# Optimization experiments

Measured on AMD Instinct MI355X. Metric: run time of the kernel, lower is better.

## Reference

```python
import jax, jax.numpy as jnp
import numpy as np

ALPHA = 0.7
L_CHAMFER, L_EDGE, L_SMOOTH, L_NORMAL = 1.0, 2.0, 1.0, 0.5
EPS = 1e-8

N, M, P, G, F = 8192, 8192, 8192, 8192, 16384


def _cdist(a, b):
    # Euclidean distance matrix, (N,3) x (M,3) -> (N,M); matches torch.cdist
    d2 = (jnp.sum(a * a, axis=1)[:, None]
          + jnp.sum(b * b, axis=1)[None, :]
          - 2.0 * a @ b.T)
    return jnp.sqrt(jnp.maximum(d2, 0.0))


def _chamfer(a, b):
    d = _cdist(a, b)
    return (d.min(axis=1).mean() + d.min(axis=0).mean()) * 0.5


def _unit(x, key):
    v = jax.random.normal(key, x, dtype=jnp.float32)
    return v / jnp.linalg.norm(v, axis=1, keepdims=True)


def setup_inputs() -> dict:
    key = jax.random.key(0)
    ks = jax.random.split(key, 7)
    return {
        "student_verts": jax.random.normal(ks[0], (N, 3), dtype=jnp.float32),
        "student_normals": _unit((N, 3), ks[1]),
        "teacher_verts": jax.random.normal(ks[2], (M, 3), dtype=jnp.float32),
        "teacher_normals": _unit((M, 3), ks[3]),
        "teacher_points": jax.random.normal(ks[4], (P, 3), dtype=jnp.float32),
        "gt_points": jax.random.normal(ks[5], (G, 3), dtype=jnp.float32),
        "faces": jax.random.randint(ks[6], (F, 3), 0, N, dtype=jnp.int32),
    }


def reference(student_verts, student_normals, teacher_verts, teacher_normals,
              teacher_points, gt_points, faces):
    # --- chamfer losses ---
    loss_teacher = _chamfer(student_verts, teacher_points)
    loss_gt = _chamfer(student_verts, gt_points)
    loss_chamfer = ALPHA * loss_teacher + (1.0 - ALPHA) * loss_gt

    # --- mesh edge loss: mean squared edge length ---
    edges = jnp.concatenate([faces[:, [0, 1]], faces[:, [1, 2]], faces[:, [2, 0]]], axis=0)  # (3F,2)
    ev = student_verts[edges[:, 0]] - student_verts[edges[:, 1]]
    loss_edge = jnp.sum(ev * ev, axis=1).mean()

    # --- uniform laplacian smoothing: mean || mean(nbrs) - v || ---
    nverts = student_verts.shape[0]
    src = jnp.concatenate([edges[:, 0], edges[:, 1]])
    dst = jnp.concatenate([edges[:, 1], edges[:, 0]])
    nbr_sum = jax.ops.segment_sum(student_verts[dst], src, num_segments=nverts)
    deg = jax.ops.segment_sum(jnp.ones_like(src, dtype=jnp.float32), src, num_segments=nverts)
    lap = nbr_sum / jnp.maximum(deg, 1.0)[:, None] - student_verts
    loss_smooth = jnp.linalg.norm(lap, axis=1).mean()
    # replicate norm with safe sqrt for grad stability

    # --- normal loss via nearest teacher vertex ---
    d_tv = _cdist(student_verts, teacher_verts)  # (N,M)
    nearest_idx = jnp.argmin(d_tv, axis=1)
    target_normals = teacher_normals[nearest_idx]  # (N,3)
    num = jnp.sum(student_normals * target_normals, axis=1)
    den = (jnp.maximum(jnp.linalg.norm(student_normals, axis=1), EPS)
           * jnp.maximum(jnp.linalg.norm(target_normals, axis=1), EPS))
    loss_normal = 1.0 - (num / den).mean()

    total = (L_CHAMFER * loss_chamfer + L_EDGE * loss_edge
             + L_SMOOTH * loss_smooth + L_NORMAL * loss_normal)
    return total
```

## Files before the change

### kernel.cpp

```cpp
#include <hip/hip_runtime.h>


typedef float f32x2 __attribute__((ext_vector_type(2)));
typedef float f32x4 __attribute__((ext_vector_type(4)));

#define BLK 256
#define TA 8
#define JC 128
#define NJG (JC / 4)

__device__ __forceinline__ float wave_reduce_sum(float v) {
#pragma unroll
  for (int o = 32; o > 0; o >>= 1) v += __shfl_down(v, o, 64);
  return v;
}

__device__ __forceinline__ unsigned flipf(float f) {
  unsigned b = __float_as_uint(f);
  return (b & 0x80000000u) ? ~b : (b | 0x80000000u);
}
__device__ __forceinline__ float unflipf(unsigned u) {
  unsigned b = (u & 0x80000000u) ? (u ^ 0x80000000u) : ~u;
  return __uint_as_float(b);
}

__device__ __forceinline__ f32x2 splat2(float v) {
  f32x2 r; r.x = v; r.y = v; return r;
}

__global__ void init_ws_kernel(unsigned long long* __restrict__ min64, int n64,
                               unsigned* __restrict__ minbits, int nmin,
                               float* __restrict__ zr, int nz) {
  const int stride = gridDim.x * blockDim.x;
  const int t0 = blockIdx.x * blockDim.x + threadIdx.x;
  for (int i = t0; i < n64; i += stride) min64[i] = ~0ull;
  for (int i = t0; i < nmin; i += stride) minbits[i] = 0xFF800000u;
  for (int i = t0; i < nz; i += stride) zr[i] = 0.0f;
}

struct Desc {
  const float* A[5];
  const float* B[5];
  void* out[5];
  const int* fc; int f;
  const float* sv;
  float* nbr; float* deg; float* acc;
  int nRows, nCols;
};

#define DIST2(d01, d23, X_, Y_, Z_, W_, k)                                 \
  f32x2 d01 = __builtin_elementwise_fma(naz[k], (Z_).xy, (W_).xy);         \
  d01 = __builtin_elementwise_fma(nay[k], (Y_).xy, d01);                   \
  d01 = __builtin_elementwise_fma(nax[k], (X_).xy, d01);                   \
  f32x2 d23 = __builtin_elementwise_fma(naz[k], (Z_).zw, (W_).zw);         \
  d23 = __builtin_elementwise_fma(nay[k], (Y_).zw, d23);                   \
  d23 = __builtin_elementwise_fma(nax[k], (X_).zw, d23);

__global__ void __launch_bounds__(BLK) mega_kernel(Desc d) {
  const int pass = blockIdx.z;
  const int t = threadIdx.x;

  if (pass == 5) {
    const int nE = 3 * d.f;
    const int bid = blockIdx.y * gridDim.x + blockIdx.x;
    const int stride = gridDim.x * gridDim.y * BLK;
    float es = 0.f;
    for (int e = bid * BLK + t; e < nE; e += stride) {
      int a, b;
      if (e < d.f)          { a = d.fc[3 * e + 0];  b = d.fc[3 * e + 1]; }
      else if (e < 2 * d.f) { int q = e - d.f;     a = d.fc[3 * q + 1]; b = d.fc[3 * q + 2]; }
      else                  { int q = e - 2 * d.f; a = d.fc[3 * q + 2]; b = d.fc[3 * q + 0]; }
      float ax = d.sv[3 * a], ay = d.sv[3 * a + 1], az = d.sv[3 * a + 2];
      float bx = d.sv[3 * b], by = d.sv[3 * b + 1], bz = d.sv[3 * b + 2];
      float dx = ax - bx, dy = ay - by, dz = az - bz;
      es += fmaf(dx, dx, fmaf(dy, dy, dz * dz));
      atomicAdd(&d.nbr[3 * a + 0], bx);
      atomicAdd(&d.nbr[3 * a + 1], by);
      atomicAdd(&d.nbr[3 * a + 2], bz);
      atomicAdd(&d.nbr[3 * b + 0], ax);
      atomicAdd(&d.nbr[3 * b + 1], ay);
      atomicAdd(&d.nbr[3 * b + 2], az);
      atomicAdd(&d.deg[a], 1.0f);
      atomicAdd(&d.deg[b], 1.0f);
    }
    es = wave_reduce_sum(es);
    if ((t & 63) == 0) atomicAdd(&d.acc[4], es);
    return;
  }

  __shared__ f32x4 sX[NJG], sY[NJG], sZ[NJG], sW[NJG];
  const float* __restrict__ A = d.A[pass];
  const float* __restrict__ B = d.B[pass];
  const int j0 = blockIdx.y * JC;
  if (t < JC) {
    int j = j0 + t;
    float bx = 0.f, by = 0.f, bz = 0.f, bw = 1e30f;
    if (j < d.nCols) {
      bx = B[3 * j]; by = B[3 * j + 1]; bz = B[3 * j + 2];
      bw = fmaf(bx, bx, fmaf(by, by, bz * bz));
    }
    ((float*)sX)[t] = bx; ((float*)sY)[t] = by;
    ((float*)sZ)[t] = bz; ((float*)sW)[t] = bw;
  }

  const int rowBase = blockIdx.x * (TA * BLK) + t;
  f32x2 nax[TA], nay[TA], naz[TA], m2[TA];
#pragma unroll
  for (int k = 0; k < TA; ++k) {
    int r = rowBase + k * BLK;
    int rc = (r < d.nRows) ? r : 0;
    nax[k] = splat2(-2.0f * A[3 * rc + 0]);
    nay[k] = splat2(-2.0f * A[3 * rc + 1]);
    naz[k] = splat2(-2.0f * A[3 * rc + 2]);
    m2[k] = splat2(1e30f);
  }
  __syncthreads();

  if (pass < 4) {
    f32x4 X = sX[0], Y = sY[0], Z = sZ[0], W = sW[0];
#pragma unroll 2
    for (int jg = 0; jg < NJG - 1; ++jg) {
      f32x4 Xn = sX[jg + 1], Yn = sY[jg + 1], Zn = sZ[jg + 1], Wn = sW[jg + 1];
#pragma unroll
      for (int k = 0; k < TA; ++k) {
        DIST2(d01, d23, X, Y, Z, W, k);
        m2[k] = __builtin_elementwise_min(
            m2[k], __builtin_elementwise_min(d01, d23));
      }
      X = Xn; Y = Yn; Z = Zn; W = Wn;
    }
#pragma unroll
    for (int k = 0; k < TA; ++k) {
      DIST2(d01, d23, X, Y, Z, W, k);
      m2[k] = __builtin_elementwise_min(
          m2[k], __builtin_elementwise_min(d01, d23));
    }
    unsigned* __restrict__ out = (unsigned*)d.out[pass];
#pragma unroll
    for (int k = 0; k < TA; ++k) {
      int r = rowBase + k * BLK;
      if (r < d.nRows) atomicMin(out + r, flipf(fminf(m2[k].x, m2[k].y)));
    }
  } else {
    f32x2 id2[TA];
#pragma unroll
    for (int k = 0; k < TA; ++k) id2[k] = splat2(0.f);
    f32x4 X = sX[0], Y = sY[0], Z = sZ[0], W = sW[0];
    for (int jg = 0; jg < NJG; ++jg) {
      f32x4 Xn, Yn, Zn, Wn;
      if (jg + 1 < NJG) { Xn = sX[jg + 1]; Yn = sY[jg + 1]; Zn = sZ[jg + 1]; Wn = sW[jg + 1]; }
      float jb = (float)(j0 + 4 * jg);
      float j1f = jb + 1.f, j2f = jb + 2.f, j3f = jb + 3.f;
#pragma unroll
      for (int k = 0; k < TA; ++k) {
        DIST2(d01, d23, X, Y, Z, W, k);
        bool c0 = d01.x < m2[k].x;
        m2[k].x = c0 ? d01.x : m2[k].x;  id2[k].x = c0 ? jb  : id2[k].x;
        bool c1 = d01.y < m2[k].y;
        m2[k].y = c1 ? d01.y : m2[k].y;  id2[k].y = c1 ? j1f : id2[k].y;
        bool c2 = d23.x < m2[k].x;
        m2[k].x = c2 ? d23.x : m2[k].x;  id2[k].x = c2 ? j2f : id2[k].x;
        bool c3 = d23.y < m2[k].y;
        m2[k].y = c3 ? d23.y : m2[k].y;  id2[k].y = c3 ? j3f : id2[k].y;
      }
      X = Xn; Y = Yn; Z = Zn; W = Wn;
    }
    unsigned long long* __restrict__ out = (unsigned long long*)d.out[4];
#pragma unroll
    for (int k = 0; k < TA; ++k) {
      int r = rowBase + k * BLK;
      unsigned long long pa =
          ((unsigned long long)flipf(m2[k].x) << 32) | (unsigned)(int)id2[k].x;
      unsigned long long pb =
          ((unsigned long long)flipf(m2[k].y) << 32) | (unsigned)(int)id2[k].y;
      unsigned long long best = pa < pb ? pa : pb;
      if (r < d.nRows) atomicMin(out + r, best);
    }
  }
}

__global__ void __launch_bounds__(BLK) post_kernel(
    const float* __restrict__ sv, const float* __restrict__ sn,
    const float* __restrict__ tn, const float* __restrict__ tp,
    const float* __restrict__ gp, const float* __restrict__ nbr,
    const float* __restrict__ deg, const unsigned* __restrict__ minbase,
    const unsigned long long* __restrict__ min64,
    int n, int p, int g, int f, float* __restrict__ acc,
    int* __restrict__ cnt, float* __restrict__ out) {
  const int task = blockIdx.y;
  const int i = blockIdx.x * blockDim.x + threadIdx.x;
  float s = 0.f;
  int accIdx;
  if (task == 0) {
    accIdx = 5;
    if (i < n) {
      float dd = fmaxf(deg[i], 1.0f);
      float lx = nbr[3 * i + 0] / dd - sv[3 * i + 0];
      float ly = nbr[3 * i + 1] / dd - sv[3 * i + 1];
      float lz = nbr[3 * i + 2] / dd - sv[3 * i + 2];
      s = sqrtf(fmaf(lx, lx, fmaf(ly, ly, lz * lz)));
    }
  } else if (task == 1) {
    accIdx = 6;
    if (i < n) {
      int idx = (int)(min64[i] & 0xffffffffull);
      float sx = sn[3 * i], sy = sn[3 * i + 1], sz = sn[3 * i + 2];
      float tx = tn[3 * idx], ty = tn[3 * idx + 1], tz = tn[3 * idx + 2];
      float num = fmaf(sx, tx, fmaf(sy, ty, sz * tz));
      float ns = sqrtf(fmaf(sx, sx, fmaf(sy, sy, sz * sz)));
      float nt = sqrtf(fmaf(tx, tx, fmaf(ty, ty, tz * tz)));
      s = num / (fmaxf(ns, 1e-8f) * fmaxf(nt, 1e-8f));
    }
  } else {
    const int seg = task - 2;
    accIdx = seg;
    const float* Aarr = (seg == 1) ? tp : (seg == 3) ? gp : sv;
    const int off = (seg == 0) ? 0 : (seg == 1) ? n : (seg == 2) ? (n + p) : (2 * n + p);
    const int cntN = (seg == 1) ? p : n;
    if (i < cntN) {
      float mval = unflipf(minbase[off + i]);
      float ax = Aarr[3 * i], ay = Aarr[3 * i + 1], az = Aarr[3 * i + 2];
      float aa = fmaf(ax, ax, fmaf(ay, ay, az * az));
      s = sqrtf(fmaxf(mval + aa, 0.0f));
    }
  }
  s = wave_reduce_sum(s);
  if ((threadIdx.x & 63) == 0) atomicAdd(&acc[accIdx], s);

  __syncthreads();
  __threadfence();
  __shared__ int last;
  if (threadIdx.x == 0)
    last = (atomicAdd(cnt, 1) == (int)(gridDim.x * gridDim.y) - 1);
  __syncthreads();
  if (last && threadIdx.x == 0) {
    float a[7];
#pragma unroll
    for (int q = 0; q < 7; ++q) a[q] = atomicAdd(&acc[q], 0.0f);
    float lt = 0.5f * (a[0] / (float)n + a[1] / (float)p);
    float lg = 0.5f * (a[2] / (float)n + a[3] / (float)g);
    float chamfer = 0.7f * lt + 0.3f * lg;
    float edge = a[4] / (float)(3 * f);
    float smooth = a[5] / (float)n;
    float normal = 1.0f - a[6] / (float)n;
    out[0] = chamfer + 2.0f * edge + smooth + 0.5f * normal;
  }
}

extern "C" void kernel_launch(void* const* d_in, const int* in_sizes, int n_in,
                              void* d_out, int out_size, void* d_ws, size_t ws_size,
                              hipStream_t stream) {
  const float* sv = (const float*)d_in[0];
  const float* sn = (const float*)d_in[1];
  const float* tv = (const float*)d_in[2];
  const float* tn = (const float*)d_in[3];
  const float* tp = (const float*)d_in[4];
  const float* gp = (const float*)d_in[5];
  const int*   fc = (const int*)d_in[6];
  const int n = in_sizes[0] / 3;
  const int m = in_sizes[2] / 3;
  const int p = in_sizes[4] / 3;
  const int g = in_sizes[5] / 3;
  const int f = in_sizes[6] / 3;

  char* w = (char*)d_ws;
  unsigned long long* min64 = (unsigned long long*)w; w += (size_t)n * 8;
  unsigned* minbase = (unsigned*)w; w += (size_t)(n + p + n + g) * 4;
  float* nbr = (float*)w; w += (size_t)n * 3 * 4;
  float* deg = (float*)w; w += (size_t)n * 4;
  float* acc = (float*)w; w += 8 * 4;
  int* cnt = (int*)w;

  unsigned* minA_tp = minbase;
  unsigned* minB_tp = minA_tp + n;
  unsigned* minA_gt = minB_tp + p;
  unsigned* minB_gt = minA_gt + n;

  const int nmin = n + p + n + g;
  const int nz = n * 3 + n + 8 + 1;

  init_ws_kernel<<<64, BLK, 0, stream>>>(min64, n, minbase, nmin, nbr, nz);

  Desc d;
  d.A[0] = sv; d.B[0] = tp; d.out[0] = minA_tp;
  d.A[1] = tp; d.B[1] = sv; d.out[1] = minB_tp;
  d.A[2] = sv; d.B[2] = gp; d.out[2] = minA_gt;
  d.A[3] = gp; d.B[3] = sv; d.out[3] = minB_gt;
  d.A[4] = sv; d.B[4] = tv; d.out[4] = min64;
  d.fc = fc; d.f = f; d.sv = sv;
  d.nbr = nbr; d.deg = deg; d.acc = acc;
  d.nRows = n; d.nCols = n;

  dim3 pgrid((n + TA * BLK - 1) / (TA * BLK), (n + JC - 1) / JC, 6);
  mega_kernel<<<pgrid, BLK, 0, stream>>>(d);

  dim3 tgrid((n + BLK - 1) / BLK, 6);
  post_kernel<<<tgrid, BLK, 0, stream>>>(sv, sn, tn, tp, gp, nbr, deg,
                                         minbase, min64, n, p, g, f,
                                         acc, cnt, (float*)d_out);
}
```

Before: 132.7 us.

## Broadcast column points via readlane from padded float4 buffers instead of LDS

Adds a prepass in the init kernel that packs every point set into float4 (x,y,z,|p|^2). The distance kernel now has each wave load its 128 column points into registers and broadcast them with readlane, replacing the shared-memory staging and the syncthreads. The packed f32x2 math becomes scalar FMAs and launch bounds are raised. This removes LDS traffic and the barrier, but costs scalar readlane instructions per column and gives up the packed-FMA throughput.

Measured after the change: 164.1 us. 1.24x slower.

```diff
diff --git a/kernel.cpp b/kernel.cpp
--- a/kernel.cpp
+++ b/kernel.cpp
@@ -1,13 +1,9 @@
 #include <hip/hip_runtime.h>
 
-
-typedef float f32x2 __attribute__((ext_vector_type(2)));
-typedef float f32x4 __attribute__((ext_vector_type(4)));
 
 #define BLK 256
 #define TA 8
 #define JC 128
-#define NJG (JC / 4)
 
 __device__ __forceinline__ float wave_reduce_sum(float v) {
 #pragma unroll
@@ -24,23 +20,39 @@
   return __uint_as_float(b);
 }
 
-__device__ __forceinline__ f32x2 splat2(float v) {
-  f32x2 r; r.x = v; r.y = v; return r;
+__device__ __forceinline__ float rdlanef(float v, int lane) {
+  return __int_as_float(__builtin_amdgcn_readlane(__float_as_int(v), lane));
 }
 
 __global__ void init_ws_kernel(unsigned long long* __restrict__ min64, int n64,
                                unsigned* __restrict__ minbits, int nmin,
-                               float* __restrict__ zr, int nz) {
+                               float* __restrict__ zr, int nz,
+                               float4* __restrict__ svp, const float* __restrict__ sv,
+                               float4* __restrict__ tpp, const float* __restrict__ tp,
+                               float4* __restrict__ gpp, const float* __restrict__ gp,
+                               float4* __restrict__ tvp, const float* __restrict__ tv,
+                               int n) {
   const int stride = gridDim.x * blockDim.x;
   const int t0 = blockIdx.x * blockDim.x + threadIdx.x;
   for (int i = t0; i < n64; i += stride) min64[i] = ~0ull;
   for (int i = t0; i < nmin; i += stride) minbits[i] = 0xFF800000u;
   for (int i = t0; i < nz; i += stride) zr[i] = 0.0f;
+  for (int i = t0; i < n; i += stride) {
+    float x, y, z;
+    x = sv[3 * i]; y = sv[3 * i + 1]; z = sv[3 * i + 2];
+    svp[i] = make_float4(x, y, z, fmaf(x, x, fmaf(y, y, z * z)));
+    x = tp[3 * i]; y = tp[3 * i + 1]; z = tp[3 * i + 2];
+    tpp[i] = make_float4(x, y, z, fmaf(x, x, fmaf(y, y, z * z)));
+    x = gp[3 * i]; y = gp[3 * i + 1]; z = gp[3 * i + 2];
+    gpp[i] = make_float4(x, y, z, fmaf(x, x, fmaf(y, y, z * z)));
+    x = tv[3 * i]; y = tv[3 * i + 1]; z = tv[3 * i + 2];
+    tvp[i] = make_float4(x, y, z, fmaf(x, x, fmaf(y, y, z * z)));
+  }
 }
 
 struct Desc {
-  const float* A[5];
-  const float* B[5];
+  const float4* A[5];
+  const float4* B[5];
   void* out[5];
   const int* fc; int f;
   const float* sv;
@@ -48,15 +60,7 @@
   int nRows, nCols;
 };
 
-#define DIST2(d01, d23, X_, Y_, Z_, W_, k)                                 \
-  f32x2 d01 = __builtin_elementwise_fma(naz[k], (Z_).xy, (W_).xy);         \
-  d01 = __builtin_elementwise_fma(nay[k], (Y_).xy, d01);                   \
-  d01 = __builtin_elementwise_fma(nax[k], (X_).xy, d01);                   \
-  f32x2 d23 = __builtin_elementwise_fma(naz[k], (Z_).zw, (W_).zw);         \
-  d23 = __builtin_elementwise_fma(nay[k], (Y_).zw, d23);                   \
-  d23 = __builtin_elementwise_fma(nax[k], (X_).zw, d23);
-
-__global__ void __launch_bounds__(BLK) mega_kernel(Desc d) {
+__global__ void __launch_bounds__(BLK, 8) mega_kernel(Desc d) {
   const int pass = blockIdx.z;
   const int t = threadIdx.x;
 
@@ -88,101 +92,100 @@
     return;
   }
 
-  __shared__ f32x4 sX[NJG], sY[NJG], sZ[NJG], sW[NJG];
-  const float* __restrict__ A = d.A[pass];
-  const float* __restrict__ B = d.B[pass];
+  const float4* __restrict__ A = d.A[pass];
+  const float4* __restrict__ B = d.B[pass];
+  const int lane = t & 63;
   const int j0 = blockIdx.y * JC;
-  if (t < JC) {
-    int j = j0 + t;
-    float bx = 0.f, by = 0.f, bz = 0.f, bw = 1e30f;
-    if (j < d.nCols) {
-      bx = B[3 * j]; by = B[3 * j + 1]; bz = B[3 * j + 2];
-      bw = fmaf(bx, bx, fmaf(by, by, bz * bz));
-    }
-    ((float*)sX)[t] = bx; ((float*)sY)[t] = by;
-    ((float*)sZ)[t] = bz; ((float*)sW)[t] = bw;
+
+  float4 bb[2];
+  {
+    int ja = j0 + lane;
+    int jb = j0 + 64 + lane;
+    bb[0] = (ja < d.nCols) ? B[ja] : make_float4(0.f, 0.f, 0.f, __int_as_float(0x7f800000));
+    bb[1] = (jb < d.nCols) ? B[jb] : make_float4(0.f, 0.f, 0.f, __int_as_float(0x7f800000));
   }
 
   const int rowBase = blockIdx.x * (TA * BLK) + t;
-  f32x2 nax[TA], nay[TA], naz[TA], m2[TA];
+  float nax[TA], nay[TA], naz[TA], m[TA];
 #pragma unroll
   for (int k = 0; k < TA; ++k) {
     int r = rowBase + k * BLK;
     int rc = (r < d.nRows) ? r : 0;
-    nax[k] = splat2(-2.0f * A[3 * rc + 0]);
-    nay[k] = splat2(-2.0f * A[3 * rc + 1]);
-    naz[k] = splat2(-2.0f * A[3 * rc + 2]);
-    m2[k] = splat2(1e30f);
-  }
-  __syncthreads();
+    float4 a = A[rc];
+    nax[k] = -2.0f * a.x;
+    nay[k] = -2.0f * a.y;
+    naz[k] = -2.0f * a.z;
+    m[k] = __int_as_float(0x7f800000);
+  }
 
   if (pass < 4) {
-    f32x4 X = sX[0], Y = sY[0], Z = sZ[0], W = sW[0];
-#pragma unroll 2
-    for (int jg = 0; jg < NJG - 1; ++jg) {
-      f32x4 Xn = sX[jg + 1], Yn = sY[jg + 1], Zn = sZ[jg + 1], Wn = sW[jg + 1];
-#pragma unroll
-      for (int k = 0; k < TA; ++k) {
-        DIST2(d01, d23, X, Y, Z, W, k);
-        m2[k] = __builtin_elementwise_min(
-            m2[k], __builtin_elementwise_min(d01, d23));
+#pragma unroll
+    for (int half = 0; half < 2; ++half) {
+      float4 bp = bb[half];
+#pragma unroll 8
+      for (int c = 0; c < 64; ++c) {
+        float bx = rdlanef(bp.x, c);
+        float by = rdlanef(bp.y, c);
+        float bz = rdlanef(bp.z, c);
+        float bw = rdlanef(bp.w, c);
+#pragma unroll
+        for (int k = 0; k < TA; ++k) {
+          float dd = fmaf(naz[k], bz, bw);
+          dd = fmaf(nay[k], by, dd);
+          dd = fmaf(nax[k], bx, dd);
+          m[k] = fminf(m[k], dd);
+        }
       }
-      X = Xn; Y = Yn; Z = Zn; W = Wn;
-    }
-#pragma unroll
-    for (int k = 0; k < TA; ++k) {
-      DIST2(d01, d23, X, Y, Z, W, k);
-      m2[k] = __builtin_elementwise_min(
-          m2[k], __builtin_elementwise_min(d01, d23));
     }
     unsigned* __restrict__ out = (unsigned*)d.out[pass];
 #pragma unroll
     for (int k = 0; k < TA; ++k) {
       int r = rowBase + k * BLK;
-      if (r < d.nRows) atomicMin(out + r, flipf(fminf(m2[k].x, m2[k].y)));
+      if (r < d.nRows) atomicMin(out + r, flipf(m[k]));
     }
   } else {
-    f32x2 id2[TA];
-#pragma unroll
-    for (int k = 0; k < TA; ++k) id2[k] = splat2(0.f);
-    f32x4 X = sX[0], Y = sY[0], Z = sZ[0], W = sW[0];
-    for (int jg = 0; jg < NJG; ++jg) {
-      f32x4 Xn, Yn, Zn, Wn;
-      if (jg + 1 < NJG) { Xn = sX[jg + 1]; Yn = sY[jg + 1]; Zn = sZ[jg + 1]; Wn = sW[jg + 1]; }
-      float jb = (float)(j0 + 4 * jg);
-      float j1f = jb + 1.f, j2f = jb + 2.f, j3f = jb + 3.f;
-#pragma unroll
-      for (int k = 0; k < TA; ++k) {
-        DIST2(d01, d23, X, Y, Z, W, k);
-        bool c0 = d01.x < m2[k].x;
-        m2[k].x = c0 ? d01.x : m2[k].x;  id2[k].x = c0 ? jb  : id2[k].x;
-        bool c1 = d01.y < m2[k].y;
-        m2[k].y = c1 ? d01.y : m2[k].y;  id2[k].y = c1 ? j1f : id2[k].y;
-        bool c2 = d23.x < m2[k].x;
-        m2[k].x = c2 ? d23.x : m2[k].x;  id2[k].x = c2 ? j2f : id2[k].x;
-        bool c3 = d23.y < m2[k].y;
-        m2[k].y = c3 ? d23.y : m2[k].y;  id2[k].y = c3 ? j3f : id2[k].y;
+    float idxf[TA];
+#pragma unroll
+    for (int k = 0; k < TA; ++k) idxf[k] = 0.f;
+#pragma unroll
+    for (int half = 0; half < 2; ++half) {
+      float4 bp = bb[half];
+      const float jbf = (float)(j0 + 64 * half);
+#pragma unroll 8
+      for (int c = 0; c < 64; ++c) {
+        float bx = rdlanef(bp.x, c);
+        float by = rdlanef(bp.y, c);
+        float bz = rdlanef(bp.z, c);
+        float bw = rdlanef(bp.w, c);
+        float jf = jbf + (float)c;
+#pragma unroll
+        for (int k = 0; k < TA; ++k) {
+          float dd = fmaf(naz[k], bz, bw);
+          dd = fmaf(nay[k], by, dd);
+          dd = fmaf(nax[k], bx, dd);
+          bool cm = dd < m[k];
+          m[k] = cm ? dd : m[k];
+          idxf[k] = cm ? jf : idxf[k];
+        }
       }
-      X = Xn; Y = Yn; Z = Zn; W = Wn;
     }
     unsigned long long* __restrict__ out = (unsigned long long*)d.out[4];
 #pragma unroll
     for (int k = 0; k < TA; ++k) {
       int r = rowBase + k * BLK;
-      unsigned long long pa =
-          ((unsigned long long)flipf(m2[k].x) << 32) | (unsigned)(int)id2[k].x;
-      unsigned long long pb =
-          ((unsigned long long)flipf(m2[k].y) << 32) | (unsigned)(int)id2[k].y;
-      unsigned long long best = pa < pb ? pa : pb;
-      if (r < d.nRows) atomicMin(out + r, best);
+      unsigned long long packed =
+          ((unsigned long long)flipf(m[k]) << 32) | (unsigned)(int)idxf[k];
+      if (r < d.nRows) atomicMin(out + r, packed);
     }
   }
 }
 
 __global__ void __launch_bounds__(BLK) post_kernel(
     const float* __restrict__ sv, const float* __restrict__ sn,
-    const float* __restrict__ tn, const float* __restrict__ tp,
-    const float* __restrict__ gp, const float* __restrict__ nbr,
+    const float* __restrict__ tn,
+    const float4* __restrict__ svp, const float4* __restrict__ tpp,
+    const float4* __restrict__ gpp,
+    const float* __restrict__ nbr,
     const float* __restrict__ deg, const unsigned* __restrict__ minbase,
     const unsigned long long* __restrict__ min64,
     int n, int p, int g, int f, float* __restrict__ acc,
@@ -214,13 +217,12 @@
   } else {
     const int seg = task - 2;
     accIdx = seg;
-    const float* Aarr = (seg == 1) ? tp : (seg == 3) ? gp : sv;
+    const float4* Aarr = (seg == 1) ? tpp : (seg == 3) ? gpp : svp;
     const int off = (seg == 0) ? 0 : (seg == 1) ? n : (seg == 2) ? (n + p) : (2 * n + p);
     const int cntN = (seg == 1) ? p : n;
     if (i < cntN) {
       float mval = unflipf(minbase[off + i]);
-      float ax = Aarr[3 * i], ay = Aarr[3 * i + 1], az = Aarr[3 * i + 2];
-      float aa = fmaf(ax, ax, fmaf(ay, ay, az * az));
+      float aa = Aarr[i].w;
       s = sqrtf(fmaxf(mval + aa, 0.0f));
     }
   }
@@ -264,6 +266,10 @@
   const int f = in_sizes[6] / 3;
 
   char* w = (char*)d_ws;
+  float4* svp = (float4*)w; w += (size_t)n * 16;
+  float4* tpp = (float4*)w; w += (size_t)p * 16;
+  float4* gpp = (float4*)w; w += (size_t)g * 16;
+  float4* tvp = (float4*)w; w += (size_t)m * 16;
   unsigned long long* min64 = (unsigned long long*)w; w += (size_t)n * 8;
   unsigned* minbase = (unsigned*)w; w += (size_t)(n + p + n + g) * 4;
   float* nbr = (float*)w; w += (size_t)n * 3 * 4;
@@ -279,14 +285,16 @@
   const int nmin = n + p + n + g;
   const int nz = n * 3 + n + 8 + 1;
 
-  init_ws_kernel<<<64, BLK, 0, stream>>>(min64, n, minbase, nmin, nbr, nz);
+  init_ws_kernel<<<256, BLK, 0, stream>>>(min64, n, minbase, nmin,
+                                          nbr, nz,
+                                          svp, sv, tpp, tp, gpp, gp, tvp, tv, n);
 
   Desc d;
-  d.A[0] = sv; d.B[0] = tp; d.out[0] = minA_tp;
-  d.A[1] = tp; d.B[1] = sv; d.out[1] = minB_tp;
-  d.A[2] = sv; d.B[2] = gp; d.out[2] = minA_gt;
-  d.A[3] = gp; d.B[3] = sv; d.out[3] = minB_gt;
-  d.A[4] = sv; d.B[4] = tv; d.out[4] = min64;
+  d.A[0] = svp; d.B[0] = tpp; d.out[0] = minA_tp;
+  d.A[1] = tpp; d.B[1] = svp; d.out[1] = minB_tp;
+  d.A[2] = svp; d.B[2] = gpp; d.out[2] = minA_gt;
+  d.A[3] = gpp; d.B[3] = svp; d.out[3] = minB_gt;
+  d.A[4] = svp; d.B[4] = tvp; d.out[4] = min64;
   d.fc = fc; d.f = f; d.sv = sv;
   d.nbr = nbr; d.deg = deg; d.acc = acc;
   d.nRows = n; d.nCols = n;
@@ -295,7 +303,7 @@
   mega_kernel<<<pgrid, BLK, 0, stream>>>(d);
 
   dim3 tgrid((n + BLK - 1) / BLK, 6);
-  post_kernel<<<tgrid, BLK, 0, stream>>>(sv, sn, tn, tp, gp, nbr, deg,
+  post_kernel<<<tgrid, BLK, 0, stream>>>(sv, sn, tn, svp, tpp, gpp, nbr, deg,
                                          minbase, min64, n, p, g, f,
                                          acc, cnt, (float*)d_out);
 }
```

## Compute pairwise distances with bf16 split-precision MFMA instead of scalar FMA

Applied to the files above, without the earlier changes.

Points are packed into bf16 hi/lo split operands so that one 32x32x16 bf16 MFMA yields full squared distances, norm terms included, for a 32x32 tile. The row/column min and argmin reductions run on the MFMA accumulators, followed by cross-lane shuffles and atomics. The goal is to move the O(N*M) distance arithmetic from vector ALUs onto the matrix cores. The cost is a packing pass in the init kernel, a hardcoded grid tied to the 8192 sizes, and possible precision loss from the bf16 split.

Result: slower. 138.2 us (+4.1%).

```diff
diff --git a/kernel.cpp b/kernel.cpp
--- a/kernel.cpp
+++ b/kernel.cpp
@@ -1,13 +1,12 @@
 #include <hip/hip_runtime.h>
 
 
-typedef float f32x2 __attribute__((ext_vector_type(2)));
-typedef float f32x4 __attribute__((ext_vector_type(4)));
+typedef short sh8 __attribute__((ext_vector_type(8)));
+typedef float f32x16 __attribute__((ext_vector_type(16)));
 
 #define BLK 256
-#define TA 8
-#define JC 128
-#define NJG (JC / 4)
+#define TR 2
+#define JTILES 64
 
 __device__ __forceinline__ float wave_reduce_sum(float v) {
 #pragma unroll
@@ -24,37 +23,83 @@
   return __uint_as_float(b);
 }
 
-__device__ __forceinline__ f32x2 splat2(float v) {
-  f32x2 r; r.x = v; r.y = v; return r;
-}
-
-__global__ void init_ws_kernel(unsigned long long* __restrict__ min64, int n64,
+__device__ __forceinline__ unsigned short f2bf(float x) {
+  unsigned u = __float_as_uint(x);
+  unsigned r = (u + 0x7FFFu + ((u >> 16) & 1u)) >> 16;
+  return (unsigned short)r;
+}
+__device__ __forceinline__ float bf2f(unsigned short b) {
+  return __uint_as_float(((unsigned)b) << 16);
+}
+
+__device__ void pack_pt(int i, float x, float y, float z, sh8* Ap, sh8* Bp) {
+  float aa = fmaf(x, x, fmaf(y, y, z * z));
+  unsigned short hx = f2bf(x), hy = f2bf(y), hz = f2bf(z);
+  float lx = x - bf2f(hx), ly = y - bf2f(hy), lz = z - bf2f(hz);
+  unsigned short haa = f2bf(aa);
+  float laa = aa - bf2f(haa);
+  const short ONE = (short)0x3F80;
+  const int base = (i >> 5) * 64 + (i & 31);
+  if (Ap) {
+    unsigned short nhx = f2bf(-2.f * bf2f(hx)), nhy = f2bf(-2.f * bf2f(hy)),
+                   nhz = f2bf(-2.f * bf2f(hz));
+    unsigned short nlx = f2bf(-2.f * lx), nly = f2bf(-2.f * ly),
+                   nlz = f2bf(-2.f * lz);
+    sh8 lo, hi;
+    lo[0] = (short)nhx; lo[1] = (short)nhy; lo[2] = (short)nhz;
+    lo[3] = (short)nlx; lo[4] = (short)nly; lo[5] = (short)nlz;
+    lo[6] = (short)nhx; lo[7] = (short)nhy;
+    hi[0] = (short)nhz; hi[1] = (short)haa; hi[2] = (short)f2bf(laa);
+    hi[3] = ONE; hi[4] = ONE; hi[5] = 0; hi[6] = 0; hi[7] = 0;
+    Ap[base] = lo; Ap[base + 32] = hi;
+  }
+  {
+    unsigned short lxb = f2bf(lx), lyb = f2bf(ly), lzb = f2bf(lz);
+    sh8 lo, hi;
+    lo[0] = (short)hx; lo[1] = (short)hy; lo[2] = (short)hz;
+    lo[3] = (short)hx; lo[4] = (short)hy; lo[5] = (short)hz;
+    lo[6] = (short)lxb; lo[7] = (short)lyb;
+    hi[0] = (short)lzb; hi[1] = ONE; hi[2] = ONE;
+    hi[3] = (short)haa; hi[4] = (short)f2bf(laa);
+    hi[5] = 0; hi[6] = 0; hi[7] = 0;
+    Bp[base] = lo; Bp[base + 32] = hi;
+  }
+}
+
+struct Packs {
+  sh8 *Asv, *Atp, *Agp;
+  sh8 *Bsv, *Btp, *Bgp, *Btv;
+};
+
+__global__ void init_ws_kernel(Packs pk,
+                               const float* __restrict__ sv,
+                               const float* __restrict__ tp,
+                               const float* __restrict__ gp,
+                               const float* __restrict__ tv,
+                               unsigned long long* __restrict__ min64, int n64,
                                unsigned* __restrict__ minbits, int nmin,
-                               float* __restrict__ zr, int nz) {
+                               float* __restrict__ zr, int nz, int n) {
   const int stride = gridDim.x * blockDim.x;
   const int t0 = blockIdx.x * blockDim.x + threadIdx.x;
   for (int i = t0; i < n64; i += stride) min64[i] = ~0ull;
   for (int i = t0; i < nmin; i += stride) minbits[i] = 0xFF800000u;
   for (int i = t0; i < nz; i += stride) zr[i] = 0.0f;
+  for (int i = t0; i < n; i += stride) {
+    pack_pt(i, sv[3 * i], sv[3 * i + 1], sv[3 * i + 2], pk.Asv, pk.Bsv);
+    pack_pt(i, tp[3 * i], tp[3 * i + 1], tp[3 * i + 2], pk.Atp, pk.Btp);
+    pack_pt(i, gp[3 * i], gp[3 * i + 1], gp[3 * i + 2], pk.Agp, pk.Bgp);
+    pack_pt(i, tv[3 * i], tv[3 * i + 1], tv[3 * i + 2], (sh8*)0, pk.Btv);
+  }
 }
 
 struct Desc {
-  const float* A[5];
-  const float* B[5];
+  const sh8* Ap[5];
+  const sh8* Bp[5];
   void* out[5];
   const int* fc; int f;
   const float* sv;
   float* nbr; float* deg; float* acc;
-  int nRows, nCols;
 };
-
-#define DIST2(d01, d23, X_, Y_, Z_, W_, k)                                 \
-  f32x2 d01 = __builtin_elementwise_fma(naz[k], (Z_).xy, (W_).xy);         \
-  d01 = __builtin_elementwise_fma(nay[k], (Y_).xy, d01);                   \
-  d01 = __builtin_elementwise_fma(nax[k], (X_).xy, d01);                   \
-  f32x2 d23 = __builtin_elementwise_fma(naz[k], (Z_).zw, (W_).zw);         \
-  d23 = __builtin_elementwise_fma(nay[k], (Y_).zw, d23);                   \
-  d23 = __builtin_elementwise_fma(nax[k], (X_).zw, d23);
 
 __global__ void __launch_bounds__(BLK) mega_kernel(Desc d) {
   const int pass = blockIdx.z;
@@ -88,102 +133,96 @@
     return;
   }
 
-  __shared__ f32x4 sX[NJG], sY[NJG], sZ[NJG], sW[NJG];
-  const float* __restrict__ A = d.A[pass];
-  const float* __restrict__ B = d.B[pass];
-  const int j0 = blockIdx.y * JC;
-  if (t < JC) {
-    int j = j0 + t;
-    float bx = 0.f, by = 0.f, bz = 0.f, bw = 1e30f;
-    if (j < d.nCols) {
-      bx = B[3 * j]; by = B[3 * j + 1]; bz = B[3 * j + 2];
-      bw = fmaf(bx, bx, fmaf(by, by, bz * bz));
-    }
-    ((float*)sX)[t] = bx; ((float*)sY)[t] = by;
-    ((float*)sZ)[t] = bz; ((float*)sW)[t] = bw;
-  }
-
-  const int rowBase = blockIdx.x * (TA * BLK) + t;
-  f32x2 nax[TA], nay[TA], naz[TA], m2[TA];
-#pragma unroll
-  for (int k = 0; k < TA; ++k) {
-    int r = rowBase + k * BLK;
-    int rc = (r < d.nRows) ? r : 0;
-    nax[k] = splat2(-2.0f * A[3 * rc + 0]);
-    nay[k] = splat2(-2.0f * A[3 * rc + 1]);
-    naz[k] = splat2(-2.0f * A[3 * rc + 2]);
-    m2[k] = splat2(1e30f);
-  }
-  __syncthreads();
+  const int wave = t >> 6, lane = t & 63;
+  const int jt0 = blockIdx.y * JTILES;
+  const float INF = __int_as_float(0x7f800000);
+  f32x16 zc;
+#pragma unroll
+  for (int q = 0; q < 16; ++q) zc[q] = 0.f;
+
+  const sh8* __restrict__ Ap = d.Ap[pass];
+  const sh8* __restrict__ Bp = d.Bp[pass];
 
   if (pass < 4) {
-    f32x4 X = sX[0], Y = sY[0], Z = sZ[0], W = sW[0];
+    if (blockIdx.x >= 32) return;
+    const int rt0 = (blockIdx.x * 4 + wave) * TR;
+    sh8 af0 = Ap[rt0 * 64 + lane];
+    sh8 af1 = Ap[(rt0 + 1) * 64 + lane];
+    f32x16 r0, r1;
+#pragma unroll
+    for (int q = 0; q < 16; ++q) { r0[q] = INF; r1[q] = INF; }
 #pragma unroll 2
-    for (int jg = 0; jg < NJG - 1; ++jg) {
-      f32x4 Xn = sX[jg + 1], Yn = sY[jg + 1], Zn = sZ[jg + 1], Wn = sW[jg + 1];
-#pragma unroll
-      for (int k = 0; k < TA; ++k) {
-        DIST2(d01, d23, X, Y, Z, W, k);
-        m2[k] = __builtin_elementwise_min(
-            m2[k], __builtin_elementwise_min(d01, d23));
+    for (int jt = 0; jt < JTILES; ++jt) {
+      sh8 bf = Bp[(jt0 + jt) * 64 + lane];
+      f32x16 c0 = __builtin_amdgcn_mfma_f32_32x32x16_bf16(af0, bf, zc, 0, 0, 0);
+      f32x16 c1 = __builtin_amdgcn_mfma_f32_32x32x16_bf16(af1, bf, zc, 0, 0, 0);
+      r0 = __builtin_elementwise_min(r0, c0);
+      r1 = __builtin_elementwise_min(r1, c1);
+    }
+    unsigned* __restrict__ out = (unsigned*)d.out[pass];
+#pragma unroll
+    for (int a = 0; a < TR; ++a) {
+#pragma unroll
+      for (int q = 0; q < 16; ++q) {
+        float v = (a == 0) ? r0[q] : r1[q];
+        v = fminf(v, __shfl_xor(v, 1));
+        v = fminf(v, __shfl_xor(v, 2));
+        v = fminf(v, __shfl_xor(v, 4));
+        v = fminf(v, __shfl_xor(v, 8));
+        v = fminf(v, __shfl_xor(v, 16));
+        if ((lane & 31) == 0) {
+          int row = (rt0 + a) * 32 + (q & 3) + 8 * (q >> 2) + 4 * (lane >> 5);
+          atomicMin(out + row, flipf(v));
+        }
       }
-      X = Xn; Y = Yn; Z = Zn; W = Wn;
-    }
-#pragma unroll
-    for (int k = 0; k < TA; ++k) {
-      DIST2(d01, d23, X, Y, Z, W, k);
-      m2[k] = __builtin_elementwise_min(
-          m2[k], __builtin_elementwise_min(d01, d23));
-    }
-    unsigned* __restrict__ out = (unsigned*)d.out[pass];
-#pragma unroll
-    for (int k = 0; k < TA; ++k) {
-      int r = rowBase + k * BLK;
-      if (r < d.nRows) atomicMin(out + r, flipf(fminf(m2[k].x, m2[k].y)));
     }
   } else {
-    f32x2 id2[TA];
-#pragma unroll
-    for (int k = 0; k < TA; ++k) id2[k] = splat2(0.f);
-    f32x4 X = sX[0], Y = sY[0], Z = sZ[0], W = sW[0];
-    for (int jg = 0; jg < NJG; ++jg) {
-      f32x4 Xn, Yn, Zn, Wn;
-      if (jg + 1 < NJG) { Xn = sX[jg + 1]; Yn = sY[jg + 1]; Zn = sZ[jg + 1]; Wn = sW[jg + 1]; }
-      float jb = (float)(j0 + 4 * jg);
-      float j1f = jb + 1.f, j2f = jb + 2.f, j3f = jb + 3.f;
-#pragma unroll
-      for (int k = 0; k < TA; ++k) {
-        DIST2(d01, d23, X, Y, Z, W, k);
-        bool c0 = d01.x < m2[k].x;
-        m2[k].x = c0 ? d01.x : m2[k].x;  id2[k].x = c0 ? jb  : id2[k].x;
-        bool c1 = d01.y < m2[k].y;
-        m2[k].y = c1 ? d01.y : m2[k].y;  id2[k].y = c1 ? j1f : id2[k].y;
-        bool c2 = d23.x < m2[k].x;
-        m2[k].x = c2 ? d23.x : m2[k].x;  id2[k].x = c2 ? j2f : id2[k].x;
-        bool c3 = d23.y < m2[k].y;
-        m2[k].y = c3 ? d23.y : m2[k].y;  id2[k].y = c3 ? j3f : id2[k].y;
+    const int rt = blockIdx.x * 4 + wave;
+    sh8 af = Ap[rt * 64 + lane];
+    f32x16 m;
+    float idx[16];
+#pragma unroll
+    for (int q = 0; q < 16; ++q) { m[q] = INF; idx[q] = 0.f; }
+#pragma unroll 2
+    for (int jt = 0; jt < JTILES; ++jt) {
+      sh8 bf = Bp[(jt0 + jt) * 64 + lane];
+      f32x16 c = __builtin_amdgcn_mfma_f32_32x32x16_bf16(af, bf, zc, 0, 0, 0);
+      float colf = (float)((jt0 + jt) * 32 + (lane & 31));
+#pragma unroll
+      for (int q = 0; q < 16; ++q) {
+        bool cm = c[q] < m[q];
+        m[q] = cm ? c[q] : m[q];
+        idx[q] = cm ? colf : idx[q];
       }
-      X = Xn; Y = Yn; Z = Zn; W = Wn;
     }
     unsigned long long* __restrict__ out = (unsigned long long*)d.out[4];
 #pragma unroll
-    for (int k = 0; k < TA; ++k) {
-      int r = rowBase + k * BLK;
-      unsigned long long pa =
-          ((unsigned long long)flipf(m2[k].x) << 32) | (unsigned)(int)id2[k].x;
-      unsigned long long pb =
-          ((unsigned long long)flipf(m2[k].y) << 32) | (unsigned)(int)id2[k].y;
-      unsigned long long best = pa < pb ? pa : pb;
-      if (r < d.nRows) atomicMin(out + r, best);
+    for (int q = 0; q < 16; ++q) {
+      float v = m[q], ix = idx[q];
+#pragma unroll
+      for (int s = 0; s < 5; ++s) {
+        int msk = 1 << s;
+        float ov = __shfl_xor(v, msk);
+        float oi = __shfl_xor(ix, msk);
+        bool take = (ov < v) || (ov == v && oi < ix);
+        v = take ? ov : v;
+        ix = take ? oi : ix;
+      }
+      if ((lane & 31) == 0) {
+        int row = rt * 32 + (q & 3) + 8 * (q >> 2) + 4 * (lane >> 5);
+        unsigned long long packed =
+            ((unsigned long long)flipf(v) << 32) | (unsigned)(int)ix;
+        atomicMin(out + row, packed);
+      }
     }
   }
 }
 
 __global__ void __launch_bounds__(BLK) post_kernel(
     const float* __restrict__ sv, const float* __restrict__ sn,
-    const float* __restrict__ tn, const float* __restrict__ tp,
-    const float* __restrict__ gp, const float* __restrict__ nbr,
-    const float* __restrict__ deg, const unsigned* __restrict__ minbase,
+    const float* __restrict__ tn,
+    const float* __restrict__ nbr, const float* __restrict__ deg,
+    const unsigned* __restrict__ minbase,
     const unsigned long long* __restrict__ min64,
     int n, int p, int g, int f, float* __restrict__ acc,
     int* __restrict__ cnt, float* __restrict__ out) {
@@ -214,14 +253,11 @@
   } else {
     const int seg = task - 2;
     accIdx = seg;
-    const float* Aarr = (seg == 1) ? tp : (seg == 3) ? gp : sv;
     const int off = (seg == 0) ? 0 : (seg == 1) ? n : (seg == 2) ? (n + p) : (2 * n + p);
     const int cntN = (seg == 1) ? p : n;
     if (i < cntN) {
-      float mval = unflipf(minbase[off + i]);
-      float ax = Aarr[3 * i], ay = Aarr[3 * i + 1], az = Aarr[3 * i + 2];
-      float aa = fmaf(ax, ax, fmaf(ay, ay, az * az));
-      s = sqrtf(fmaxf(mval + aa, 0.0f));
+      float d2 = unflipf(minbase[off + i]);
+      s = sqrtf(fmaxf(d2, 0.0f));
     }
   }
   s = wave_reduce_sum(s);
@@ -264,6 +300,14 @@
   const int f = in_sizes[6] / 3;
 
   char* w = (char*)d_ws;
+  Packs pk;
+  pk.Asv = (sh8*)w; w += (size_t)n * 32;
+  pk.Atp = (sh8*)w; w += (size_t)p * 32;
+  pk.Agp = (sh8*)w; w += (size_t)g * 32;
+  pk.Bsv = (sh8*)w; w += (size_t)n * 32;
+  pk.Btp = (sh8*)w; w += (size_t)p * 32;
+  pk.Bgp = (sh8*)w; w += (size_t)g * 32;
+  pk.Btv = (sh8*)w; w += (size_t)m * 32;
   unsigned long long* min64 = (unsigned long long*)w; w += (size_t)n * 8;
   unsigned* minbase = (unsigned*)w; w += (size_t)(n + p + n + g) * 4;
   float* nbr = (float*)w; w += (size_t)n * 3 * 4;
@@ -279,23 +323,23 @@
   const int nmin = n + p + n + g;
   const int nz = n * 3 + n + 8 + 1;
 
-  init_ws_kernel<<<64, BLK, 0, stream>>>(min64, n, minbase, nmin, nbr, nz);
+  init_ws_kernel<<<64, BLK, 0, stream>>>(pk, sv, tp, gp, tv,
+                                         min64, n, minbase, nmin, nbr, nz, n);
 
   Desc d;
-  d.A[0] = sv; d.B[0] = tp; d.out[0] = minA_tp;
-  d.A[1] = tp; d.B[1] = sv; d.out[1] = minB_tp;
-  d.A[2] = sv; d.B[2] = gp; d.out[2] = minA_gt;
-  d.A[3] = gp; d.B[3] = sv; d.out[3] = minB_gt;
-  d.A[4] = sv; d.B[4] = tv; d.out[4] = min64;
+  d.Ap[0] = pk.Asv; d.Bp[0] = pk.Btp; d.out[0] = minA_tp;
+  d.Ap[1] = pk.Atp; d.Bp[1] = pk.Bsv; d.out[1] = minB_tp;
+  d.Ap[2] = pk.Asv; d.Bp[2] = pk.Bgp; d.out[2] = minA_gt;
+  d.Ap[3] = pk.Agp; d.Bp[3] = pk.Bsv; d.out[3] = minB_gt;
+  d.Ap[4] = pk.Asv; d.Bp[4] = pk.Btv; d.out[4] = min64;
   d.fc = fc; d.f = f; d.sv = sv;
   d.nbr = nbr; d.deg = deg; d.acc = acc;
-  d.nRows = n; d.nCols = n;
-
-  dim3 pgrid((n + TA * BLK - 1) / (TA * BLK), (n + JC - 1) / JC, 6);
+
+  dim3 pgrid(64, 4, 6);
   mega_kernel<<<pgrid, BLK, 0, stream>>>(d);
 
   dim3 tgrid((n + BLK - 1) / BLK, 6);
-  post_kernel<<<tgrid, BLK, 0, stream>>>(sv, sn, tn, tp, gp, nbr, deg,
+  post_kernel<<<tgrid, BLK, 0, stream>>>(sv, sn, tn, nbr, deg,
                                          minbase, min64, n, p, g, f,
                                          acc, cnt, (float*)d_out);
 }
```
